# Kernel tuning notes

Measured on AMD Instinct MI355X. Metric: run time of the kernel, lower is better.

The kernel has to match this reference:

```python
import jax, jax.numpy as jnp
import numpy as np

N = 20000      # nodes
E = 320000     # edges (avg in-degree 16)
R = 100        # relation types
F = 256        # in_ent_feats == out_ent_feats == in_rel_feats
H = 8          # heads
D = F // H     # head dim = 32
HOP = 5        # PPR hops
ALPHA = 0.1
SLOPE = 0.2    # LeakyReLU negative slope


def _ln(x, g, b, eps=1e-5):
    m = x.mean(-1, keepdims=True)
    v = ((x - m) ** 2).mean(-1, keepdims=True)
    return (x - m) / jnp.sqrt(v + eps) * g + b


def setup_inputs() -> dict:
    key = jax.random.key(0)
    ks = jax.random.split(key, 12)
    s = 1.0 / np.sqrt(F)
    ent_feat = jax.random.normal(ks[0], (N, F), jnp.float32)
    rel_feat = jax.random.normal(ks[1], (R, F), jnp.float32)
    W_head = jax.random.normal(ks[2], (F, F), jnp.float32) * s
    W_tail = jax.random.normal(ks[3], (F, F), jnp.float32) * s
    W_ent = jax.random.normal(ks[4], (F, F), jnp.float32) * s
    W_rel = jax.random.normal(ks[5], (F, F), jnp.float32) * s
    attn = jax.random.normal(ks[6], (1, H, D), jnp.float32) * s
    ln_ent_g = jnp.ones((F,), jnp.float32); ln_ent_b = jnp.zeros((F,), jnp.float32)
    ln_rel_g = jnp.ones((F,), jnp.float32); ln_rel_b = jnp.zeros((F,), jnp.float32)
    ln_ff_g = jnp.ones((F,), jnp.float32); ln_ff_b = jnp.zeros((F,), jnp.float32)
    W1 = jax.random.normal(ks[7], (F, 4 * F), jnp.float32) * s
    b1 = jnp.zeros((4 * F,), jnp.float32)
    W2 = jax.random.normal(ks[8], (4 * F, F), jnp.float32) * (0.5 * s)
    b2 = jnp.zeros((F,), jnp.float32)
    src = jax.random.randint(ks[9], (E,), 0, N, dtype=jnp.int32)
    # every node must have in-degree >= 1 (DGL raises on 0-in-degree nodes)
    dst = jnp.concatenate([jnp.arange(N, dtype=jnp.int32),
                           jax.random.randint(ks[10], (E - N,), 0, N, dtype=jnp.int32)])
    rid = jax.random.randint(ks[11], (E,), 0, R, dtype=jnp.int32)
    return {"ent_feat": ent_feat, "rel_feat": rel_feat,
            "W_head": W_head, "W_tail": W_tail, "W_ent": W_ent, "W_rel": W_rel,
            "attn": attn,
            "ln_ent_g": ln_ent_g, "ln_ent_b": ln_ent_b,
            "ln_rel_g": ln_rel_g, "ln_rel_b": ln_rel_b,
            "ln_ff_g": ln_ff_g, "ln_ff_b": ln_ff_b,
            "W1": W1, "b1": b1, "W2": W2, "b2": b2,
            "src": src, "dst": dst, "rid": rid}


def reference(ent_feat, rel_feat, W_head, W_tail, W_ent, W_rel, attn,
              ln_ent_g, ln_ent_b, ln_rel_g, ln_rel_b, ln_ff_g, ln_ff_b,
              W1, b1, W2, b2, src, dst, rid):
    n = ent_feat.shape[0]
    x = _ln(ent_feat, ln_ent_g, ln_ent_b)                 # [N,F]
    fh = (x @ W_head).reshape(n, H, D)                    # 'eh'
    ftl = (x @ W_tail).reshape(n, H, D)                   # 'et'
    fen = (x @ W_ent).reshape(n, H, D)                    # 'ft'
    r = _ln(rel_feat, ln_rel_g, ln_rel_b)
    fr = (r @ W_rel).reshape(-1, H, D)[rid]               # [E,H,D]
    # relational edge attention score
    e = jax.nn.leaky_relu(fh[src] * ftl[dst] * fr, SLOPE)
    e = (e * attn).sum(-1)                                # [E,H]
    # e_mul_v with log in-degree, scaled by head_dim
    deg = jax.ops.segment_sum(jnp.ones((src.shape[0],), e.dtype), dst, num_segments=n)
    e = e * (jnp.log(deg)[dst])[:, None] / D
    # edge softmax over incoming edges of each dst node, per head
    m = jax.lax.stop_gradient(jax.ops.segment_max(e, dst, num_segments=n))
    ex = jnp.exp(e - m[dst])
    denom = jax.ops.segment_sum(ex, dst, num_segments=n)
    a = ex / denom[dst]                                   # [E,H]
    # PPR-style diffusion aggregation
    feat0 = fen
    feat = fen
    for _ in range(HOP):
        msg = feat[src] * a[:, :, None]                   # [E,H,D]
        agg = jax.ops.segment_sum(msg, dst, num_segments=n)
        feat = (1.0 - ALPHA) * agg + ALPHA * feat0
    # residual (Identity since in_ent_feats == out_ent_feats)
    rst = feat + ent_feat.reshape(n, H, D)
    rst = rst.reshape(n, F)
    # position-wise feed-forward with pre-LN and residual
    y = _ln(rst, ln_ff_g, ln_ff_b)
    ff = jax.nn.relu(y @ W1 + b1) @ W2 + b2
    return ff + rst
```

## Files before the change

kernel.cpp:

```cpp
#include <hip/hip_runtime.h>

#define N_NODES 20000
#define N_EDGES 320000
#define N_REL   100
#define FDIM    256
#define NHEAD   8
#define HDIM    32
#define SCAN_BLOCKS ((N_NODES + 255) / 256)

using short8 = __attribute__((ext_vector_type(8))) short;
using f32x4  = __attribute__((ext_vector_type(4))) float;

__device__ inline unsigned short f2bf(float f) {
    union { float f; unsigned int u; } v; v.f = f;
    unsigned int r = v.u + 0x7fff + ((v.u >> 16) & 1);
    return (unsigned short)(r >> 16);
}
__device__ inline float bf2f(unsigned short u) {
    union { unsigned int i; float f; } v; v.i = ((unsigned int)u) << 16; return v.f;
}
__device__ inline float4 bf4(ushort4 u) {
    return make_float4(bf2f(u.x), bf2f(u.y), bf2f(u.z), bf2f(u.w));
}
__device__ inline void unpack8(float* d, uint4 u) {
    union { unsigned int u; float f; } t;
    t.u = u.x << 16;         d[0] = t.f;
    t.u = u.x & 0xffff0000u; d[1] = t.f;
    t.u = u.y << 16;         d[2] = t.f;
    t.u = u.y & 0xffff0000u; d[3] = t.f;
    t.u = u.z << 16;         d[4] = t.f;
    t.u = u.z & 0xffff0000u; d[5] = t.f;
    t.u = u.w << 16;         d[6] = t.f;
    t.u = u.w & 0xffff0000u; d[7] = t.f;
}
__device__ inline void fma8(float* acc, uint4 u, float w) {
    union { unsigned int u; float f; } t;
    t.u = u.x << 16;         acc[0] += w * t.f;
    t.u = u.x & 0xffff0000u; acc[1] += w * t.f;
    t.u = u.y << 16;         acc[2] += w * t.f;
    t.u = u.y & 0xffff0000u; acc[3] += w * t.f;
    t.u = u.z << 16;         acc[4] += w * t.f;
    t.u = u.z & 0xffff0000u; acc[5] += w * t.f;
    t.u = u.w << 16;         acc[6] += w * t.f;
    t.u = u.w & 0xffff0000u; acc[7] += w * t.f;
}
__device__ __forceinline__ void g2lds16(const unsigned short* g, unsigned short* l) {
    __builtin_amdgcn_global_load_lds(
        (const __attribute__((address_space(1))) unsigned int*)g,
        (__attribute__((address_space(3))) unsigned int*)l,
        16, 0, 0);
}

__device__ inline void xcd_tile(int* m0, int* n0, int tm, int tn) {
    int nwg  = gridDim.x * gridDim.y;
    int wgid = blockIdx.x + blockIdx.y * gridDim.x;
    int q = nwg >> 3, r = nwg & 7;
    int xcd = wgid & 7, pos = wgid >> 3;
    int nid = (xcd < r ? xcd * (q + 1) : r * (q + 1) + (xcd - r) * q) + pos;
    int gy = gridDim.y;
    int bx = nid / gy;
    int by = nid - bx * gy;
    *m0 = bx * tm;
    *n0 = by * tn;
}

__global__ __launch_bounds__(64) void ln_fused_kernel(
    const float* __restrict__ ent, const float* __restrict__ rel,
    const float* __restrict__ ge, const float* __restrict__ be,
    const float* __restrict__ gr, const float* __restrict__ br,
    unsigned short* __restrict__ xb, unsigned short* __restrict__ rlnb)
{
    int row = blockIdx.x;
    const float *in, *g, *b; unsigned short* out; int r;
    if (row < N_NODES) { in = ent; g = ge; b = be; out = xb;   r = row; }
    else               { in = rel; g = gr; b = br; out = rlnb; r = row - N_NODES; }
    int tid = threadIdx.x;
    const float4 v = *(const float4*)(in + (size_t)r * FDIM + tid * 4);
    float s = v.x + v.y + v.z + v.w;
    float q = v.x * v.x + v.y * v.y + v.z * v.z + v.w * v.w;
    #pragma unroll
    for (int d = 1; d < 64; d <<= 1) { s += __shfl_xor(s, d); q += __shfl_xor(q, d); }
    float mean = s * (1.0f / FDIM);
    float var  = q * (1.0f / FDIM) - mean * mean;
    float inv  = rsqrtf(var + 1e-5f);
    float4 gg = *(const float4*)(g + tid * 4);
    float4 bb = *(const float4*)(b + tid * 4);
    ushort4 o;
    o.x = f2bf((v.x - mean) * inv * gg.x + bb.x);
    o.y = f2bf((v.y - mean) * inv * gg.y + bb.y);
    o.z = f2bf((v.z - mean) * inv * gg.z + bb.z);
    o.w = f2bf((v.w - mean) * inv * gg.w + bb.w);
    *(ushort4*)(out + (size_t)r * FDIM + tid * 4) = o;
}

__global__ __launch_bounds__(64) void rst_ln_kernel(
    const unsigned short* __restrict__ feat, const float* __restrict__ ent,
    const float* __restrict__ g, const float* __restrict__ b,
    float* __restrict__ rst, unsigned short* __restrict__ y)
{
    int row = blockIdx.x;
    int tid = threadIdx.x;
    const float4 f = bf4(*(const ushort4*)(feat + (size_t)row * FDIM + tid * 4));
    const float4 e = *(const float4*)(ent + (size_t)row * FDIM + tid * 4);
    float4 r;
    r.x = f.x + e.x; r.y = f.y + e.y; r.z = f.z + e.z; r.w = f.w + e.w;
    *(float4*)(rst + (size_t)row * FDIM + tid * 4) = r;
    float s = r.x + r.y + r.z + r.w;
    float q = r.x * r.x + r.y * r.y + r.z * r.z + r.w * r.w;
    #pragma unroll
    for (int d = 1; d < 64; d <<= 1) { s += __shfl_xor(s, d); q += __shfl_xor(q, d); }
    float mean = s * (1.0f / FDIM);
    float var  = q * (1.0f / FDIM) - mean * mean;
    float inv  = rsqrtf(var + 1e-5f);
    float4 gg = *(const float4*)(g + tid * 4);
    float4 bb = *(const float4*)(b + tid * 4);
    ushort4 o;
    o.x = f2bf((r.x - mean) * inv * gg.x + bb.x);
    o.y = f2bf((r.y - mean) * inv * gg.y + bb.y);
    o.z = f2bf((r.z - mean) * inv * gg.z + bb.z);
    o.w = f2bf((r.w - mean) * inv * gg.w + bb.w);
    *(ushort4*)(y + (size_t)row * FDIM + tid * 4) = o;
}

__global__ void transpose_all_kernel(
    const float* __restrict__ Wh, const float* __restrict__ Wt_,
    const float* __restrict__ We, const float* __restrict__ Wr,
    const float* __restrict__ W1, const float* __restrict__ W2,
    unsigned short* __restrict__ WtP, unsigned short* __restrict__ WtR,
    unsigned short* __restrict__ W1t, unsigned short* __restrict__ W2t)
{
    int idx = blockIdx.x * 256 + threadIdx.x;
    if (idx < 196608) {
        int seg = idx >> 16, r = idx & 65535;
        const float* W = (seg == 0) ? Wh : (seg == 1) ? Wt_ : We;
        int n = r >> 8, k = r & 255;
        WtP[idx] = f2bf(W[k * 256 + n]);
    } else if (idx < 262144) {
        int r = idx - 196608;
        int n = r >> 8, k = r & 255;
        WtR[r] = f2bf(Wr[k * 256 + n]);
    } else if (idx < 524288) {
        int r = idx - 262144;
        int n = r >> 8, k = r & 255;
        W1t[r] = f2bf(W1[k * 1024 + n]);
    } else if (idx < 786432) {
        int r = idx - 524288;
        int n = r >> 10, k = r & 1023;
        W2t[r] = f2bf(W2[k * 256 + n]);
    }
}

__global__ __launch_bounds__(256) void mfma_gemm_bt(
    const unsigned short* __restrict__ A, const unsigned short* __restrict__ Bt,
    const float* __restrict__ bias, const float* __restrict__ add,
    float* __restrict__ Cf, unsigned short* __restrict__ Cb,
    int M, int K, int N, int relu)
{
    __shared__ unsigned short As[2][128 * 32];
    __shared__ unsigned short Bs[2][128 * 32];
    int tid  = threadIdx.x;
    int wave = tid >> 6, lane = tid & 63;
    int quad = lane >> 4, l16 = lane & 15;
    int m0, n0;
    xcd_tile(&m0, &n0, 128, 128);
    int wr = (wave >> 1) * 64, wc = (wave & 1) * 64;

    f32x4 acc[4][4] = {};

    int cA = tid, cB = tid + 256;
    int rA0 = cA >> 2, kA0 = (cA & 3) * 8;
    int rB0 = cB >> 2, kB0 = (cB & 3) * 8;
    int rA = m0 + rA0; if (rA >= M) rA = M - 1;
    int rB = m0 + rB0; if (rB >= M) rB = M - 1;
    const unsigned short* gA0 = A + (size_t)rA * K + kA0;
    const unsigned short* gA1 = A + (size_t)rB * K + kB0;
    const unsigned short* gB0 = Bt + (size_t)(n0 + rA0) * K + kA0;
    const unsigned short* gB1 = Bt + (size_t)(n0 + rB0) * K + kB0;

    g2lds16(gA0, As[0] + cA * 8);
    g2lds16(gA1, As[0] + cB * 8);
    g2lds16(gB0, Bs[0] + cA * 8);
    g2lds16(gB1, Bs[0] + cB * 8);
    __syncthreads();

    int cur = 0;
    for (int k0 = 0; k0 < K; k0 += 32) {
        int k1 = k0 + 32;
        if (k1 < K) {
            int nb = cur ^ 1;
            g2lds16(gA0 + k1, As[nb] + cA * 8);
            g2lds16(gA1 + k1, As[nb] + cB * 8);
            g2lds16(gB0 + k1, Bs[nb] + cA * 8);
            g2lds16(gB1 + k1, Bs[nb] + cB * 8);
        }
        short8 af[4], bfr[4];
        #pragma unroll
        for (int i = 0; i < 4; ++i)
            af[i] = *(const short8*)(As[cur] + (wr + i * 16 + l16) * 32 + quad * 8);
        #pragma unroll
        for (int j = 0; j < 4; ++j)
            bfr[j] = *(const short8*)(Bs[cur] + (wc + j * 16 + l16) * 32 + quad * 8);
        #pragma unroll
        for (int i = 0; i < 4; ++i)
            #pragma unroll
            for (int j = 0; j < 4; ++j)
                acc[i][j] = __builtin_amdgcn_mfma_f32_16x16x32_bf16(
                    af[i], bfr[j], acc[i][j], 0, 0, 0);
        __syncthreads();
        cur ^= 1;
    }

    #pragma unroll
    for (int i = 0; i < 4; ++i) {
        #pragma unroll
        for (int j = 0; j < 4; ++j) {
            int col = n0 + wc + j * 16 + l16;
            float bsv = bias ? bias[col] : 0.0f;
            #pragma unroll
            for (int r = 0; r < 4; ++r) {
                int row = m0 + wr + i * 16 + quad * 4 + r;
                if (row < M) {
                    float v = acc[i][j][r] + bsv;
                    if (relu) v = fmaxf(v, 0.0f);
                    if (add)  v += add[(size_t)row * N + col];
                    if (Cf) Cf[(size_t)row * N + col] = v;
                    else    Cb[(size_t)row * N + col] = f2bf(v);
                }
            }
        }
    }
}

__global__ __launch_bounds__(256) void mfma_gemm64_bt(
    const unsigned short* __restrict__ A, const unsigned short* __restrict__ Bt,
    const float* __restrict__ bias, const float* __restrict__ add,
    float* __restrict__ Cf, int M, int K, int N)
{
    __shared__ unsigned short As[2][64 * 32];
    __shared__ unsigned short Bs[2][128 * 32];
    int tid  = threadIdx.x;
    int wave = tid >> 6, lane = tid & 63;
    int quad = lane >> 4, l16 = lane & 15;
    int m0, n0;
    xcd_tile(&m0, &n0, 64, 128);
    int wc = wave * 32;

    f32x4 acc[4][2] = {};

    int rA0 = tid >> 2, kA0 = (tid & 3) * 8;
    int cB0 = tid, cB1 = tid + 256;
    int rB0 = cB0 >> 2, kB0 = (cB0 & 3) * 8;
    int rB1 = cB1 >> 2, kB1 = (cB1 & 3) * 8;
    int rA = m0 + rA0; if (rA >= M) rA = M - 1;
    const unsigned short* gA  = A + (size_t)rA * K + kA0;
    const unsigned short* gB0 = Bt + (size_t)(n0 + rB0) * K + kB0;
    const unsigned short* gB1 = Bt + (size_t)(n0 + rB1) * K + kB1;

    g2lds16(gA,  As[0] + tid * 8);
    g2lds16(gB0, Bs[0] + cB0 * 8);
    g2lds16(gB1, Bs[0] + cB1 * 8);
    __syncthreads();

    int cur = 0;
    for (int k0 = 0; k0 < K; k0 += 32) {
        short8 af[4], bfr[2];
        #pragma unroll
        for (int i = 0; i < 4; ++i)
            af[i] = *(const short8*)(As[cur] + (i * 16 + l16) * 32 + quad * 8);
        #pragma unroll
        for (int j = 0; j < 2; ++j)
            bfr[j] = *(const short8*)(Bs[cur] + (wc + j * 16 + l16) * 32 + quad * 8);
        int k1 = k0 + 32;
        if (k1 < K) {
            int nb = cur ^ 1;
            g2lds16(gA + k1,  As[nb] + tid * 8);
            g2lds16(gB0 + k1, Bs[nb] + cB0 * 8);
            g2lds16(gB1 + k1, Bs[nb] + cB1 * 8);
        }
        #pragma unroll
        for (int i = 0; i < 4; ++i)
            #pragma unroll
            for (int j = 0; j < 2; ++j)
                acc[i][j] = __builtin_amdgcn_mfma_f32_16x16x32_bf16(
                    af[i], bfr[j], acc[i][j], 0, 0, 0);
        __syncthreads();
        cur ^= 1;
    }

    #pragma unroll
    for (int i = 0; i < 4; ++i) {
        #pragma unroll
        for (int j = 0; j < 2; ++j) {
            int col = n0 + wc + j * 16 + l16;
            float bsv = bias ? bias[col] : 0.0f;
            #pragma unroll
            for (int r = 0; r < 4; ++r) {
                int row = m0 + i * 16 + quad * 4 + r;
                if (row < M) {
                    float v = acc[i][j][r] + bsv;
                    if (add) v += add[(size_t)row * N + col];
                    Cf[(size_t)row * N + col] = v;
                }
            }
        }
    }
}

__global__ void count_kernel(const int* __restrict__ dst, int* __restrict__ deg, int E)
{
    int i = blockIdx.x * blockDim.x + threadIdx.x;
    if (i < E) atomicAdd(&deg[dst[i]], 1);
}

__global__ __launch_bounds__(256) void scan1_kernel(
    const int* __restrict__ deg, int* __restrict__ offsets, int* __restrict__ bsum, int n)
{
    __shared__ int tmp[256];
    int tid = threadIdx.x;
    int i = blockIdx.x * 256 + tid;
    int v = (i < n) ? deg[i] : 0;
    tmp[tid] = v;
    __syncthreads();
    for (int d = 1; d < 256; d <<= 1) {
        int u = (tid >= d) ? tmp[tid - d] : 0;
        __syncthreads();
        tmp[tid] += u;
        __syncthreads();
    }
    if (i < n) offsets[i] = tmp[tid] - v;
    if (tid == 255) bsum[blockIdx.x] = tmp[255];
}

__global__ __launch_bounds__(128) void scan2_kernel(int* __restrict__ bsum, int nb)
{
    __shared__ int tmp[128];
    int tid = threadIdx.x;
    int v = (tid < nb) ? bsum[tid] : 0;
    tmp[tid] = v;
    __syncthreads();
    for (int d = 1; d < 128; d <<= 1) {
        int u = (tid >= d) ? tmp[tid - d] : 0;
        __syncthreads();
        tmp[tid] += u;
        __syncthreads();
    }
    if (tid < nb) bsum[tid] = tmp[tid] - v;
}

__global__ __launch_bounds__(256) void scan3_kernel(
    const int* __restrict__ deg, int* __restrict__ offsets,
    const int* __restrict__ bsum, int* __restrict__ cursor,
    float* __restrict__ logdeg, int n, int E)
{
    int i = blockIdx.x * 256 + threadIdx.x;
    if (i < n) {
        int o = offsets[i] + bsum[blockIdx.x];
        offsets[i] = o;
        cursor[i]  = o;
        logdeg[i]  = logf((float)deg[i]);
    }
    if (i == 0) offsets[n] = E;
}

__global__ void scatter_kernel(const int* __restrict__ dst, const int* __restrict__ src,
                               const int* __restrict__ rid, int* __restrict__ cursor,
                               int* __restrict__ csr_src, int* __restrict__ csr_rid, int E)
{
    int i = blockIdx.x * blockDim.x + threadIdx.x;
    if (i < E) {
        int p = atomicAdd(&cursor[dst[i]], 1);
        csr_src[p] = src[i];
        csr_rid[p] = rid[i];
    }
}

__global__ __launch_bounds__(256) void score_hop1_kernel(
    const unsigned short* __restrict__ proj,
    const unsigned short* __restrict__ frel,
    const float* __restrict__ attn,
    const int* __restrict__ csr_src, const int* __restrict__ csr_rid,
    const int* __restrict__ offsets, const float* __restrict__ logdeg,
    float* __restrict__ csr_a, float* __restrict__ invd,
    unsigned short* __restrict__ fout, int n)
{
    int node = blockIdx.x * 4 + (threadIdx.x >> 6);
    if (node >= n) return;
    int tid = threadIdx.x & 63;
    int g = tid >> 4, li = tid & 15;
    int start = offsets[node], end = offsets[node + 1];
    float scale = logdeg[node] * (1.0f / 32.0f);

    float tv[16], at[16];
    {
        const unsigned short* tp = proj + (size_t)node * 768 + 256 + li * 16;
        uint4 a0 = *(const uint4*)tp, a1 = *(const uint4*)(tp + 8);
        unpack8(tv, a0); unpack8(tv + 8, a1);
        const float4* ap = (const float4*)(attn + li * 16);
        float4 f;
        f = ap[0]; at[0] = f.x; at[1] = f.y; at[2]  = f.z; at[3]  = f.w;
        f = ap[1]; at[4] = f.x; at[5] = f.y; at[6]  = f.z; at[7]  = f.w;
        f = ap[2]; at[8] = f.x; at[9] = f.y; at[10] = f.z; at[11] = f.w;
        f = ap[3]; at[12] = f.x; at[13] = f.y; at[14] = f.z; at[15] = f.w;
    }

    float acc[16] = {};
    float denom = 0.f;
    for (int p = start; p < end; p += 4) {
        int e = p + g;
        bool va = e < end;
        int q = va ? e : end - 1;
        int s = csr_src[q], r = csr_rid[q];
        const unsigned short* hp = proj + (size_t)s * 768 + li * 16;
        const unsigned short* rp = frel + (size_t)r * FDIM + li * 16;
        uint4 h0 = *(const uint4*)hp,        h1 = *(const uint4*)(hp + 8);
        uint4 r0 = *(const uint4*)rp,        r1 = *(const uint4*)(rp + 8);
        uint4 e0 = *(const uint4*)(hp + 512), e1 = *(const uint4*)(hp + 520);
        float hv[16], rv[16];
        unpack8(hv, h0); unpack8(hv + 8, h1);
        unpack8(rv, r0); unpack8(rv + 8, r1);
        float sum = 0.f;
        #pragma unroll
        for (int k = 0; k < 16; ++k) {
            float m = hv[k] * tv[k] * rv[k];
            m = (m > 0.f) ? m : 0.2f * m;
            sum += m * at[k];
        }
        sum += __shfl_xor(sum, 1);
        float ex = va ? __expf(sum * scale) : 0.f;
        if (va && ((li & 1) == 0))
            csr_a[(size_t)e * NHEAD + (li >> 1)] = ex;
        denom += ex;
        fma8(acc + 0, e0, ex);
        fma8(acc + 8, e1, ex);
    }
    denom += __shfl_xor(denom, 16);
    denom += __shfl_xor(denom, 32);
    #pragma unroll
    for (int k = 0; k < 16; ++k) {
        acc[k] += __shfl_xor(acc[k], 16);
        acc[k] += __shfl_xor(acc[k], 32);
    }
    float wn = 1.0f / denom;
    if (g == 0 && (li & 1) == 0)
        invd[node * NHEAD + (li >> 1)] = wn;
    if (g == 0) {
        const unsigned short* f0p = proj + (size_t)node * 768 + 512 + li * 16;
        uint4 f0a = *(const uint4*)(f0p);
        uint4 f0b = *(const uint4*)(f0p + 8);
        float f0[16];
        unpack8(f0, f0a); unpack8(f0 + 8, f0b);
        unsigned short o[16];
        #pragma unroll
        for (int k = 0; k < 16; ++k)
            o[k] = f2bf(0.9f * acc[k] * wn + 0.1f * f0[k]);
        uint4* dst4 = (uint4*)(fout + (size_t)node * FDIM + li * 16);
        dst4[0] = *(uint4*)(o);
        dst4[1] = *(uint4*)(o + 8);
    }
}

__global__ __launch_bounds__(256) void diffuse_kernel(
    const unsigned short* __restrict__ fin, int fin_stride,
    const unsigned short* __restrict__ feat0,
    const float* __restrict__ a, const float* __restrict__ invd,
    const int* __restrict__ csr_src,
    const int* __restrict__ offsets, unsigned short* __restrict__ fout, int n)
{
    int node = blockIdx.x * 4 + (threadIdx.x >> 6);
    if (node >= n) return;
    int tid = threadIdx.x & 63;
    int g = tid >> 4, li = tid & 15;
    int hh = li >> 1;
    int start = offsets[node], end = offsets[node + 1];
    float wnorm = invd[node * NHEAD + hh];
    float acc[16] = {};

    for (int p = start; p < end; p += 16) {
        uint4 u0[4], u1[4]; float w[4];
        #pragma unroll
        for (int t = 0; t < 4; ++t) {
            int pe = p + t * 4 + g;
            int q = (pe < end) ? pe : end - 1;
            int s = csr_src[q];
            w[t] = (pe < end) ? a[(size_t)q * NHEAD + hh] : 0.0f;
            const unsigned short* rp = fin + (size_t)s * fin_stride + li * 16;
            u0[t] = *(const uint4*)(rp);
            u1[t] = *(const uint4*)(rp + 8);
        }
        #pragma unroll
        for (int t = 0; t < 4; ++t) {
            fma8(acc + 0, u0[t], w[t]);
            fma8(acc + 8, u1[t], w[t]);
        }
    }
    #pragma unroll
    for (int k = 0; k < 16; ++k) {
        acc[k] += __shfl_xor(acc[k], 16);
        acc[k] += __shfl_xor(acc[k], 32);
    }
    if (g == 0) {
        const unsigned short* f0p = feat0 + (size_t)node * 768 + li * 16;
        uint4 f0a = *(const uint4*)(f0p);
        uint4 f0b = *(const uint4*)(f0p + 8);
        float f0[16];
        unpack8(f0, f0a); unpack8(f0 + 8, f0b);
        unsigned short o[16];
        #pragma unroll
        for (int k = 0; k < 16; ++k)
            o[k] = f2bf(0.9f * acc[k] * wnorm + 0.1f * f0[k]);
        uint4* dst4 = (uint4*)(fout + (size_t)node * FDIM + li * 16);
        dst4[0] = *(uint4*)(o);
        dst4[1] = *(uint4*)(o + 8);
    }
}

extern "C" void kernel_launch(void* const* d_in, const int* in_sizes, int n_in,
                              void* d_out, int out_size, void* d_ws, size_t ws_size,
                              hipStream_t stream)
{
    const float* ent_feat = (const float*)d_in[0];
    const float* rel_feat = (const float*)d_in[1];
    const float* W_head   = (const float*)d_in[2];
    const float* W_tail   = (const float*)d_in[3];
    const float* W_ent    = (const float*)d_in[4];
    const float* W_rel    = (const float*)d_in[5];
    const float* attn     = (const float*)d_in[6];
    const float* ln_ent_g = (const float*)d_in[7];
    const float* ln_ent_b = (const float*)d_in[8];
    const float* ln_rel_g = (const float*)d_in[9];
    const float* ln_rel_b = (const float*)d_in[10];
    const float* ln_ff_g  = (const float*)d_in[11];
    const float* ln_ff_b  = (const float*)d_in[12];
    const float* W1       = (const float*)d_in[13];
    const float* b1       = (const float*)d_in[14];
    const float* W2       = (const float*)d_in[15];
    const float* b2       = (const float*)d_in[16];
    const int*   src      = (const int*)d_in[17];
    const int*   dst      = (const int*)d_in[18];
    const int*   rid      = (const int*)d_in[19];
    float* out = (float*)d_out;

    char* base = (char*)d_ws;
    auto carve = [&](size_t bytes) { char* p = base; base += (bytes + 255) & ~(size_t)255; return p; };
    unsigned short* xb    = (unsigned short*)carve((size_t)N_NODES * FDIM * 2);
    unsigned short* projb = (unsigned short*)carve((size_t)N_NODES * 768 * 2);
    unsigned short* rlnb  = (unsigned short*)carve((size_t)N_REL * FDIM * 2);
    unsigned short* frelb = (unsigned short*)carve((size_t)N_REL * FDIM * 2);
    unsigned short* WtP   = (unsigned short*)carve((size_t)768 * FDIM * 2);
    unsigned short* WtR   = (unsigned short*)carve((size_t)FDIM * FDIM * 2);
    unsigned short* W1t   = (unsigned short*)carve((size_t)1024 * FDIM * 2);
    unsigned short* W2t   = (unsigned short*)carve((size_t)FDIM * 1024 * 2);
    unsigned short* hb0   = (unsigned short*)carve((size_t)N_NODES * FDIM * 2);
    unsigned short* hb1   = (unsigned short*)carve((size_t)N_NODES * FDIM * 2);
    unsigned short* yb    = (unsigned short*)carve((size_t)N_NODES * FDIM * 2);
    unsigned short* t1b   = (unsigned short*)carve((size_t)N_NODES * 1024 * 2);
    float* rst     = (float*)carve((size_t)N_NODES * FDIM * 4);
    float* csr_a   = (float*)carve(((size_t)N_EDGES * NHEAD + 256) * 4);
    float* invd    = (float*)carve((size_t)N_NODES * NHEAD * 4);
    int*   csr_src = (int*)carve((size_t)(N_EDGES + 64) * 4);
    int*   csr_rid = (int*)carve((size_t)(N_EDGES + 64) * 4);
    int*   deg     = (int*)carve((size_t)N_NODES * 4);
    float* logdeg  = (float*)carve((size_t)N_NODES * 4);
    int*   offsets = (int*)carve((size_t)(N_NODES + 1) * 4);
    int*   cursor  = (int*)carve((size_t)N_NODES * 4);
    int*   bsum    = (int*)carve((size_t)SCAN_BLOCKS * 4);

    hipMemsetAsync(deg, 0, (size_t)N_NODES * 4, stream);

    ln_fused_kernel<<<N_NODES + N_REL, 64, 0, stream>>>(
        ent_feat, rel_feat, ln_ent_g, ln_ent_b, ln_rel_g, ln_rel_b, xb, rlnb);

    transpose_all_kernel<<<786432 / 256, 256, 0, stream>>>(
        W_head, W_tail, W_ent, W_rel, W1, W2, WtP, WtR, W1t, W2t);

    dim3 gproj((N_NODES + 127) / 128, 768 / 128);
    mfma_gemm_bt<<<gproj, 256, 0, stream>>>(xb, WtP, nullptr, nullptr, nullptr, projb,
                                            N_NODES, FDIM, 768, 0);
    dim3 grel(1, FDIM / 128);
    mfma_gemm_bt<<<grel, 256, 0, stream>>>(rlnb, WtR, nullptr, nullptr, nullptr, frelb,
                                           N_REL, FDIM, FDIM, 0);

    count_kernel<<<(N_EDGES + 255) / 256, 256, 0, stream>>>(dst, deg, N_EDGES);
    scan1_kernel<<<SCAN_BLOCKS, 256, 0, stream>>>(deg, offsets, bsum, N_NODES);
    scan2_kernel<<<1, 128, 0, stream>>>(bsum, SCAN_BLOCKS);
    scan3_kernel<<<SCAN_BLOCKS, 256, 0, stream>>>(deg, offsets, bsum, cursor, logdeg,
                                                  N_NODES, N_EDGES);
    scatter_kernel<<<(N_EDGES + 255) / 256, 256, 0, stream>>>(dst, src, rid, cursor,
                                                              csr_src, csr_rid, N_EDGES);

    score_hop1_kernel<<<(N_NODES + 3) / 4, 256, 0, stream>>>(
        projb, frelb, attn, csr_src, csr_rid, offsets, logdeg,
        csr_a, invd, hb0, N_NODES);

    const unsigned short* fen = projb + 512;
    int gdif = (N_NODES + 3) / 4;
    diffuse_kernel<<<gdif, 256, 0, stream>>>(hb0, FDIM, fen, csr_a, invd, csr_src, offsets, hb1, N_NODES);
    diffuse_kernel<<<gdif, 256, 0, stream>>>(hb1, FDIM, fen, csr_a, invd, csr_src, offsets, hb0, N_NODES);
    diffuse_kernel<<<gdif, 256, 0, stream>>>(hb0, FDIM, fen, csr_a, invd, csr_src, offsets, hb1, N_NODES);
    diffuse_kernel<<<gdif, 256, 0, stream>>>(hb1, FDIM, fen, csr_a, invd, csr_src, offsets, hb0, N_NODES);

    rst_ln_kernel<<<N_NODES, 64, 0, stream>>>(hb0, ent_feat, ln_ff_g, ln_ff_b, rst, yb);

    dim3 gff1((N_NODES + 127) / 128, 1024 / 128);
    mfma_gemm_bt<<<gff1, 256, 0, stream>>>(yb, W1t, b1, nullptr, nullptr, t1b,
                                           N_NODES, FDIM, 1024, 1);
    dim3 gff2((N_NODES + 63) / 64, FDIM / 128);
    mfma_gemm64_bt<<<gff2, 256, 0, stream>>>(t1b, W2t, b2, rst, out,
                                             N_NODES, 1024, FDIM);
}
```

Baseline: 460.1 us.

## Fuse prep kernels into one launch and fold residual+LayerNorm into last diffusion hop

Merges the input LayerNorm, weight transpose/bf16 conversion, and in-degree counting into a single prep_kernel launch, with blocks partitioned by index range. The LN part now packs four rows per 256-thread block. The final diffusion hop is fused with the residual add and FFN pre-LayerNorm, so the bf16 hop output is no longer written and re-read. This also keeps the last hop's feature in fp32 for the residual instead of rounding it to bf16. The aim is fewer launches and less memory traffic, at the cost of a heavier epilogue in the last diffusion kernel.

```diff
diff --git a/kernel.cpp b/kernel.cpp
--- a/kernel.cpp
+++ b/kernel.cpp
@@ -7,6 +7,9 @@
 #define NHEAD   8
 #define HDIM    32
 #define SCAN_BLOCKS ((N_NODES + 255) / 256)
+#define LN_BLOCKS  ((N_NODES + N_REL) / 4)
+#define TR_BLOCKS  3072
+#define CNT_BLOCKS ((N_EDGES + 255) / 256)
 
 using short8 = __attribute__((ext_vector_type(8))) short;
 using f32x4  = __attribute__((ext_vector_type(4))) float;
@@ -64,89 +67,65 @@
     *n0 = by * tn;
 }
 
-__global__ __launch_bounds__(64) void ln_fused_kernel(
+__global__ __launch_bounds__(256) void prep_kernel(
     const float* __restrict__ ent, const float* __restrict__ rel,
     const float* __restrict__ ge, const float* __restrict__ be,
     const float* __restrict__ gr, const float* __restrict__ br,
-    unsigned short* __restrict__ xb, unsigned short* __restrict__ rlnb)
-{
-    int row = blockIdx.x;
-    const float *in, *g, *b; unsigned short* out; int r;
-    if (row < N_NODES) { in = ent; g = ge; b = be; out = xb;   r = row; }
-    else               { in = rel; g = gr; b = br; out = rlnb; r = row - N_NODES; }
-    int tid = threadIdx.x;
-    const float4 v = *(const float4*)(in + (size_t)r * FDIM + tid * 4);
-    float s = v.x + v.y + v.z + v.w;
-    float q = v.x * v.x + v.y * v.y + v.z * v.z + v.w * v.w;
-    #pragma unroll
-    for (int d = 1; d < 64; d <<= 1) { s += __shfl_xor(s, d); q += __shfl_xor(q, d); }
-    float mean = s * (1.0f / FDIM);
-    float var  = q * (1.0f / FDIM) - mean * mean;
-    float inv  = rsqrtf(var + 1e-5f);
-    float4 gg = *(const float4*)(g + tid * 4);
-    float4 bb = *(const float4*)(b + tid * 4);
-    ushort4 o;
-    o.x = f2bf((v.x - mean) * inv * gg.x + bb.x);
-    o.y = f2bf((v.y - mean) * inv * gg.y + bb.y);
-    o.z = f2bf((v.z - mean) * inv * gg.z + bb.z);
-    o.w = f2bf((v.w - mean) * inv * gg.w + bb.w);
-    *(ushort4*)(out + (size_t)r * FDIM + tid * 4) = o;
-}
-
-__global__ __launch_bounds__(64) void rst_ln_kernel(
-    const unsigned short* __restrict__ feat, const float* __restrict__ ent,
-    const float* __restrict__ g, const float* __restrict__ b,
-    float* __restrict__ rst, unsigned short* __restrict__ y)
-{
-    int row = blockIdx.x;
-    int tid = threadIdx.x;
-    const float4 f = bf4(*(const ushort4*)(feat + (size_t)row * FDIM + tid * 4));
-    const float4 e = *(const float4*)(ent + (size_t)row * FDIM + tid * 4);
-    float4 r;
-    r.x = f.x + e.x; r.y = f.y + e.y; r.z = f.z + e.z; r.w = f.w + e.w;
-    *(float4*)(rst + (size_t)row * FDIM + tid * 4) = r;
-    float s = r.x + r.y + r.z + r.w;
-    float q = r.x * r.x + r.y * r.y + r.z * r.z + r.w * r.w;
-    #pragma unroll
-    for (int d = 1; d < 64; d <<= 1) { s += __shfl_xor(s, d); q += __shfl_xor(q, d); }
-    float mean = s * (1.0f / FDIM);
-    float var  = q * (1.0f / FDIM) - mean * mean;
-    float inv  = rsqrtf(var + 1e-5f);
-    float4 gg = *(const float4*)(g + tid * 4);
-    float4 bb = *(const float4*)(b + tid * 4);
-    ushort4 o;
-    o.x = f2bf((r.x - mean) * inv * gg.x + bb.x);
-    o.y = f2bf((r.y - mean) * inv * gg.y + bb.y);
-    o.z = f2bf((r.z - mean) * inv * gg.z + bb.z);
-    o.w = f2bf((r.w - mean) * inv * gg.w + bb.w);
-    *(ushort4*)(y + (size_t)row * FDIM + tid * 4) = o;
-}
-
-__global__ void transpose_all_kernel(
+    unsigned short* __restrict__ xb, unsigned short* __restrict__ rlnb,
     const float* __restrict__ Wh, const float* __restrict__ Wt_,
     const float* __restrict__ We, const float* __restrict__ Wr,
     const float* __restrict__ W1, const float* __restrict__ W2,
     unsigned short* __restrict__ WtP, unsigned short* __restrict__ WtR,
-    unsigned short* __restrict__ W1t, unsigned short* __restrict__ W2t)
-{
-    int idx = blockIdx.x * 256 + threadIdx.x;
-    if (idx < 196608) {
-        int seg = idx >> 16, r = idx & 65535;
-        const float* W = (seg == 0) ? Wh : (seg == 1) ? Wt_ : We;
-        int n = r >> 8, k = r & 255;
-        WtP[idx] = f2bf(W[k * 256 + n]);
-    } else if (idx < 262144) {
-        int r = idx - 196608;
-        int n = r >> 8, k = r & 255;
-        WtR[r] = f2bf(Wr[k * 256 + n]);
-    } else if (idx < 524288) {
-        int r = idx - 262144;
-        int n = r >> 8, k = r & 255;
-        W1t[r] = f2bf(W1[k * 1024 + n]);
-    } else if (idx < 786432) {
-        int r = idx - 524288;
-        int n = r >> 10, k = r & 1023;
-        W2t[r] = f2bf(W2[k * 256 + n]);
+    unsigned short* __restrict__ W1t, unsigned short* __restrict__ W2t,
+    const int* __restrict__ dst, int* __restrict__ deg)
+{
+    int blk = blockIdx.x;
+    if (blk < LN_BLOCKS) {
+        int row = blk * 4 + (threadIdx.x >> 6);
+        if (row >= N_NODES + N_REL) return;
+        const float *in, *g, *b; unsigned short* out; int r;
+        if (row < N_NODES) { in = ent; g = ge; b = be; out = xb;   r = row; }
+        else               { in = rel; g = gr; b = br; out = rlnb; r = row - N_NODES; }
+        int tid = threadIdx.x & 63;
+        const float4 v = *(const float4*)(in + (size_t)r * FDIM + tid * 4);
+        float s = v.x + v.y + v.z + v.w;
+        float q = v.x * v.x + v.y * v.y + v.z * v.z + v.w * v.w;
+        #pragma unroll
+        for (int d = 1; d < 64; d <<= 1) { s += __shfl_xor(s, d); q += __shfl_xor(q, d); }
+        float mean = s * (1.0f / FDIM);
+        float var  = q * (1.0f / FDIM) - mean * mean;
+        float inv  = rsqrtf(var + 1e-5f);
+        float4 gg = *(const float4*)(g + tid * 4);
+        float4 bb = *(const float4*)(b + tid * 4);
+        ushort4 o;
+        o.x = f2bf((v.x - mean) * inv * gg.x + bb.x);
+        o.y = f2bf((v.y - mean) * inv * gg.y + bb.y);
+        o.z = f2bf((v.z - mean) * inv * gg.z + bb.z);
+        o.w = f2bf((v.w - mean) * inv * gg.w + bb.w);
+        *(ushort4*)(out + (size_t)r * FDIM + tid * 4) = o;
+    } else if (blk < LN_BLOCKS + TR_BLOCKS) {
+        int idx = (blk - LN_BLOCKS) * 256 + threadIdx.x;
+        if (idx < 196608) {
+            int seg = idx >> 16, r = idx & 65535;
+            const float* W = (seg == 0) ? Wh : (seg == 1) ? Wt_ : We;
+            int n = r >> 8, k = r & 255;
+            WtP[idx] = f2bf(W[k * 256 + n]);
+        } else if (idx < 262144) {
+            int r = idx - 196608;
+            int n = r >> 8, k = r & 255;
+            WtR[r] = f2bf(Wr[k * 256 + n]);
+        } else if (idx < 524288) {
+            int r = idx - 262144;
+            int n = r >> 8, k = r & 255;
+            W1t[r] = f2bf(W1[k * 1024 + n]);
+        } else {
+            int r = idx - 524288;
+            int n = r >> 10, k = r & 1023;
+            W2t[r] = f2bf(W2[k * 256 + n]);
+        }
+    } else {
+        int i = (blk - LN_BLOCKS - TR_BLOCKS) * 256 + threadIdx.x;
+        if (i < N_EDGES) atomicAdd(&deg[dst[i]], 1);
     }
 }
 
@@ -304,12 +283,6 @@
             }
         }
     }
-}
-
-__global__ void count_kernel(const int* __restrict__ dst, int* __restrict__ deg, int E)
-{
-    int i = blockIdx.x * blockDim.x + threadIdx.x;
-    if (i < E) atomicAdd(&deg[dst[i]], 1);
 }
 
 __global__ __launch_bounds__(256) void scan1_kernel(
@@ -509,6 +482,90 @@
         for (int k = 0; k < 16; ++k)
             o[k] = f2bf(0.9f * acc[k] * wnorm + 0.1f * f0[k]);
         uint4* dst4 = (uint4*)(fout + (size_t)node * FDIM + li * 16);
+        dst4[0] = *(uint4*)(o);
+        dst4[1] = *(uint4*)(o + 8);
+    }
+}
+
+__global__ __launch_bounds__(256) void diffuse_rstln_kernel(
+    const unsigned short* __restrict__ fin, int fin_stride,
+    const unsigned short* __restrict__ feat0,
+    const float* __restrict__ a, const float* __restrict__ invd,
+    const int* __restrict__ csr_src, const int* __restrict__ offsets,
+    const float* __restrict__ ent,
+    const float* __restrict__ lng, const float* __restrict__ lnb,
+    float* __restrict__ rst, unsigned short* __restrict__ y, int n)
+{
+    int node = blockIdx.x * 4 + (threadIdx.x >> 6);
+    if (node >= n) return;
+    int tid = threadIdx.x & 63;
+    int g = tid >> 4, li = tid & 15;
+    int hh = li >> 1;
+    int start = offsets[node], end = offsets[node + 1];
+    float wnorm = invd[node * NHEAD + hh];
+    float acc[16] = {};
+
+    for (int p = start; p < end; p += 16) {
+        uint4 u0[4], u1[4]; float w[4];
+        #pragma unroll
+        for (int t = 0; t < 4; ++t) {
+            int pe = p + t * 4 + g;
+            int q = (pe < end) ? pe : end - 1;
+            int s = csr_src[q];
+            w[t] = (pe < end) ? a[(size_t)q * NHEAD + hh] : 0.0f;
+            const unsigned short* rp = fin + (size_t)s * fin_stride + li * 16;
+            u0[t] = *(const uint4*)(rp);
+            u1[t] = *(const uint4*)(rp + 8);
+        }
+        #pragma unroll
+        for (int t = 0; t < 4; ++t) {
+            fma8(acc + 0, u0[t], w[t]);
+            fma8(acc + 8, u1[t], w[t]);
+        }
+    }
+    #pragma unroll
+    for (int k = 0; k < 16; ++k) {
+        acc[k] += __shfl_xor(acc[k], 16);
+        acc[k] += __shfl_xor(acc[k], 32);
+    }
+
+    const unsigned short* f0p = feat0 + (size_t)node * 768 + li * 16;
+    uint4 f0a = *(const uint4*)(f0p);
+    uint4 f0b = *(const uint4*)(f0p + 8);
+    float f0[16];
+    unpack8(f0, f0a); unpack8(f0 + 8, f0b);
+    const float* ep = ent + (size_t)node * FDIM + li * 16;
+    float4 e0 = *(const float4*)(ep),     e1 = *(const float4*)(ep + 4);
+    float4 e2 = *(const float4*)(ep + 8), e3 = *(const float4*)(ep + 12);
+    float ev[16] = { e0.x, e0.y, e0.z, e0.w, e1.x, e1.y, e1.z, e1.w,
+                     e2.x, e2.y, e2.z, e2.w, e3.x, e3.y, e3.z, e3.w };
+    float r[16];
+    #pragma unroll
+    for (int k = 0; k < 16; ++k)
+        r[k] = 0.9f * acc[k] * wnorm + 0.1f * f0[k] + ev[k];
+
+    float s = 0.f, q = 0.f;
+    #pragma unroll
+    for (int k = 0; k < 16; ++k) { s += r[k]; q += r[k] * r[k]; }
+    #pragma unroll
+    for (int d = 1; d < 16; d <<= 1) { s += __shfl_xor(s, d); q += __shfl_xor(q, d); }
+    float mean = s * (1.0f / FDIM);
+    float var  = q * (1.0f / FDIM) - mean * mean;
+    float inv  = rsqrtf(var + 1e-5f);
+
+    if (g == 0) {
+        float* rp4 = rst + (size_t)node * FDIM + li * 16;
+        *(float4*)(rp4 + 0)  = make_float4(r[0],  r[1],  r[2],  r[3]);
+        *(float4*)(rp4 + 4)  = make_float4(r[4],  r[5],  r[6],  r[7]);
+        *(float4*)(rp4 + 8)  = make_float4(r[8],  r[9],  r[10], r[11]);
+        *(float4*)(rp4 + 12) = make_float4(r[12], r[13], r[14], r[15]);
+        const float* gp = lng + li * 16;
+        const float* bp = lnb + li * 16;
+        unsigned short o[16];
+        #pragma unroll
+        for (int k = 0; k < 16; ++k)
+            o[k] = f2bf((r[k] - mean) * inv * gp[k] + bp[k]);
+        uint4* dst4 = (uint4*)(y + (size_t)node * FDIM + li * 16);
         dst4[0] = *(uint4*)(o);
         dst4[1] = *(uint4*)(o + 8);
     }
@@ -567,11 +624,10 @@
 
     hipMemsetAsync(deg, 0, (size_t)N_NODES * 4, stream);
 
-    ln_fused_kernel<<<N_NODES + N_REL, 64, 0, stream>>>(
-        ent_feat, rel_feat, ln_ent_g, ln_ent_b, ln_rel_g, ln_rel_b, xb, rlnb);
-
-    transpose_all_kernel<<<786432 / 256, 256, 0, stream>>>(
-        W_head, W_tail, W_ent, W_rel, W1, W2, WtP, WtR, W1t, W2t);
+    prep_kernel<<<LN_BLOCKS + TR_BLOCKS + CNT_BLOCKS, 256, 0, stream>>>(
+        ent_feat, rel_feat, ln_ent_g, ln_ent_b, ln_rel_g, ln_rel_b, xb, rlnb,
+        W_head, W_tail, W_ent, W_rel, W1, W2, WtP, WtR, W1t, W2t,
+        dst, deg);
 
     dim3 gproj((N_NODES + 127) / 128, 768 / 128);
     mfma_gemm_bt<<<gproj, 256, 0, stream>>>(xb, WtP, nullptr, nullptr, nullptr, projb,
@@ -580,7 +636,6 @@
     mfma_gemm_bt<<<grel, 256, 0, stream>>>(rlnb, WtR, nullptr, nullptr, nullptr, frelb,
                                            N_REL, FDIM, FDIM, 0);
 
-    count_kernel<<<(N_EDGES + 255) / 256, 256, 0, stream>>>(dst, deg, N_EDGES);
     scan1_kernel<<<SCAN_BLOCKS, 256, 0, stream>>>(deg, offsets, bsum, N_NODES);
     scan2_kernel<<<1, 128, 0, stream>>>(bsum, SCAN_BLOCKS);
     scan3_kernel<<<SCAN_BLOCKS, 256, 0, stream>>>(deg, offsets, bsum, cursor, logdeg,
@@ -597,9 +652,9 @@
     diffuse_kernel<<<gdif, 256, 0, stream>>>(hb0, FDIM, fen, csr_a, invd, csr_src, offsets, hb1, N_NODES);
     diffuse_kernel<<<gdif, 256, 0, stream>>>(hb1, FDIM, fen, csr_a, invd, csr_src, offsets, hb0, N_NODES);
     diffuse_kernel<<<gdif, 256, 0, stream>>>(hb0, FDIM, fen, csr_a, invd, csr_src, offsets, hb1, N_NODES);
-    diffuse_kernel<<<gdif, 256, 0, stream>>>(hb1, FDIM, fen, csr_a, invd, csr_src, offsets, hb0, N_NODES);
-
-    rst_ln_kernel<<<N_NODES, 64, 0, stream>>>(hb0, ent_feat, ln_ff_g, ln_ff_b, rst, yb);
+    diffuse_rstln_kernel<<<gdif, 256, 0, stream>>>(
+        hb1, FDIM, fen, csr_a, invd, csr_src, offsets,
+        ent_feat, ln_ff_g, ln_ff_b, rst, yb, N_NODES);
 
     dim3 gff1((N_NODES + 127) / 128, 1024 / 128);
     mfma_gemm_bt<<<gff1, 256, 0, stream>>>(yb, W1t, b1, nullptr, nullptr, t1b,
```

Result: no change. 456.4 us (-0.8%).
